# Kernel tuning notes

Measured on AMD Instinct MI355X. Metric: run time of the kernel, lower is better.

Reference implementation:

```python
import jax, jax.numpy as jnp
import numpy as np

N_EMBD = 512
N_HEAD = 8


def setup_inputs() -> dict:
    key = jax.random.key(0)
    k_x, k_aw, k_ab, k_pw, k_pb = jax.random.split(key, 5)
    B, T, E = 4, 2048, N_EMBD
    s = 1.0 / np.sqrt(E)
    return {
        "x": jax.random.normal(k_x, (B, T, E), dtype=jnp.float32),
        # torch Linear weight is [out, in]; store transposed for x @ W
        "c_attn_w": jax.random.uniform(k_aw, (E, 3 * E), jnp.float32, -s, s),
        "c_attn_b": jax.random.uniform(k_ab, (3 * E,), jnp.float32, -s, s),
        "c_proj_w": jax.random.uniform(k_pw, (E, E), jnp.float32, -s, s),
        "c_proj_b": jax.random.uniform(k_pb, (E,), jnp.float32, -s, s),
    }


def reference(x, c_attn_w, c_attn_b, c_proj_w, c_proj_b):
    B, T, E = x.shape
    H = N_HEAD
    D = E // H
    qkv = x @ c_attn_w + c_attn_b                      # [B,T,3E]
    q, k, v = jnp.split(qkv, 3, axis=2)
    # [B,T,E] -> [B,H,T,D]
    q = q.reshape(B, T, H, D).transpose(0, 2, 1, 3)
    k = k.reshape(B, T, H, D).transpose(0, 2, 1, 3)
    v = v.reshape(B, T, H, D).transpose(0, 2, 1, 3)
    scale = 1.0 / np.sqrt(D).astype(np.float32)
    scores = jnp.einsum("bhqd,bhkd->bhqk", q, k) * scale
    causal = jnp.tril(jnp.ones((T, T), dtype=bool))    # [T,T]
    scores = jnp.where(causal, scores, -jnp.inf)
    attn = jax.nn.softmax(scores, axis=-1)             # [B,H,T,T]
    y = jnp.einsum("bhqk,bhkd->bhqd", attn, v)         # [B,H,T,D]
    y = y.transpose(0, 2, 1, 3).reshape(B, T, E)
    return y @ c_proj_w + c_proj_b
```

## Files before the change

kernel.cpp:

```cpp
#include <hip/hip_runtime.h>
#include <math.h>

#define N_EMBD 512
#define N_HEAD 8
#define SEQ_T  2048
#define BATCH  4
#define QKV_LD 1536

typedef __attribute__((ext_vector_type(8))) short bf16x8;
typedef __attribute__((ext_vector_type(4))) float f32x4;

#define CL 0.18033688f

__device__ __forceinline__ unsigned short f2bf(float f) {
    union { float f; unsigned int u; } x; x.f = f;
    return (unsigned short)((x.u + 0x7FFFu + ((x.u >> 16) & 1u)) >> 16);
}
__device__ __forceinline__ unsigned pack_trunc(float a, float b) {
    union { float f; unsigned u; } x, y; x.f = a; y.f = b;
    return __builtin_amdgcn_perm(y.u, x.u, 0x07060302u);
}
__device__ __forceinline__ bf16x8 scale_frag(bf16x8 v, float c) {
    bf16x8 r;
    #pragma unroll
    for (int i = 0; i < 8; ++i) {
        union { unsigned u; float f; } x;
        x.u = ((unsigned)(unsigned short)v[i]) << 16;
        r[i] = (short)f2bf(x.f * c);
    }
    return r;
}

__device__ __forceinline__ void gl_lds16(const void* g, void* s) {
    __builtin_amdgcn_global_load_lds(
        (const __attribute__((address_space(1))) void*)g,
        (__attribute__((address_space(3))) void*)s, 16, 0, 0);
}

__global__ __launch_bounds__(256) void prep(
    const float* __restrict__ w1, unsigned short* __restrict__ w1t,
    const float* __restrict__ w2, unsigned short* __restrict__ w2t)
{
    __shared__ float t[32][33];
    const int bx = blockIdx.x, tid = threadIdx.x;
    const float* W; unsigned short* Wt; int N, tt, nb;
    if (bx < 768) { tt = bx;       W = w1; Wt = w1t; N = 1536; nb = 48; }
    else          { tt = bx - 768; W = w2; Wt = w2t; N = 512;  nb = 16; }
    const int n0 = (tt % nb) * 32, k0 = (tt / nb) * 32;
    const int tx = tid & 31, ty = tid >> 5;
    #pragma unroll
    for (int i = 0; i < 4; ++i)
        t[ty + i * 8][tx] = W[(size_t)(k0 + ty + i * 8) * N + n0 + tx];
    __syncthreads();
    #pragma unroll
    for (int i = 0; i < 4; ++i)
        Wt[(size_t)(n0 + ty + i * 8) * 512 + k0 + tx] = f2bf(t[tx][ty + i * 8]);
}

template <int BM, int BN, bool CVT_A, bool BF16_OUT>
__global__ __launch_bounds__(256) void gemm_mfma(
    const void* __restrict__ Asrc,
    const unsigned short* __restrict__ Bt,
    const float* __restrict__ bias,
    void* __restrict__ C, int N, int K)
{
    constexpr int WMT = BM / 32, WNT = BN / 32;
    constexpr int SA = BM * 8 / 256, SB = BN * 8 / 256;
    __shared__ unsigned short As[BM * 64];
    __shared__ unsigned short Bs[BN * 64];

    const int tid  = threadIdx.x;
    const int wave = tid >> 6, lane = tid & 63;
    const int low  = lane & 15, quad = lane >> 4;
    const int wm   = (wave & 1) * (BM / 2), wn = (wave >> 1) * (BN / 2);
    const int row0 = blockIdx.y * BM, col0 = blockIdx.x * BN;

    size_t a_src[SA]; int a_dst[SA];
    #pragma unroll
    for (int s = 0; s < SA; ++s) {
        const int p = tid + 256 * s;
        const int m = p >> 3, q = p & 7;
        a_src[s] = (size_t)(row0 + m) * K + q * 8;
        a_dst[s] = m * 64 + (q ^ (m & 7)) * 8;
    }
    size_t b_src[SB]; int b_dst[SB];
    #pragma unroll
    for (int s = 0; s < SB; ++s) {
        const int p = tid + 256 * s;
        const int m = p >> 3, q = p & 7;
        b_src[s] = (size_t)(col0 + m) * K + q * 8;
        b_dst[s] = m * 64 + (q ^ (m & 7)) * 8;
    }

    f32x4 acc[WMT][WNT];
    #pragma unroll
    for (int i = 0; i < WMT; ++i)
        #pragma unroll
        for (int j = 0; j < WNT; ++j) acc[i][j] = (f32x4){0.f, 0.f, 0.f, 0.f};

    bf16x8 ar[SA], br[SB];
    const float*          af32 = (const float*)Asrc;
    const unsigned short* a16  = (const unsigned short*)Asrc;

    #pragma unroll
    for (int s = 0; s < SA; ++s) {
        if (CVT_A) {
            const float4 f0 = *(const float4*)(af32 + a_src[s]);
            const float4 f1 = *(const float4*)(af32 + a_src[s] + 4);
            union { uint4 v; bf16x8 h; } u;
            u.v.x = pack_trunc(f0.x, f0.y); u.v.y = pack_trunc(f0.z, f0.w);
            u.v.z = pack_trunc(f1.x, f1.y); u.v.w = pack_trunc(f1.z, f1.w);
            ar[s] = u.h;
        } else {
            ar[s] = *(const bf16x8*)(a16 + a_src[s]);
        }
    }
    #pragma unroll
    for (int s = 0; s < SB; ++s) br[s] = *(const bf16x8*)(Bt + b_src[s]);

    const int NIT = K >> 6;
    for (int it = 0; it < NIT; ++it) {
        __syncthreads();
        #pragma unroll
        for (int s = 0; s < SA; ++s) *(bf16x8*)&As[a_dst[s]] = ar[s];
        #pragma unroll
        for (int s = 0; s < SB; ++s) *(bf16x8*)&Bs[b_dst[s]] = br[s];
        __syncthreads();

        if (it + 1 < NIT) {
            const int ko = (it + 1) * 64;
            #pragma unroll
            for (int s = 0; s < SA; ++s) {
                if (CVT_A) {
                    const float4 f0 = *(const float4*)(af32 + a_src[s] + ko);
                    const float4 f1 = *(const float4*)(af32 + a_src[s] + ko + 4);
                    union { uint4 v; bf16x8 h; } u;
                    u.v.x = pack_trunc(f0.x, f0.y); u.v.y = pack_trunc(f0.z, f0.w);
                    u.v.z = pack_trunc(f1.x, f1.y); u.v.w = pack_trunc(f1.z, f1.w);
                    ar[s] = u.h;
                } else {
                    ar[s] = *(const bf16x8*)(a16 + a_src[s] + ko);
                }
            }
            #pragma unroll
            for (int s = 0; s < SB; ++s) br[s] = *(const bf16x8*)(Bt + b_src[s] + ko);
        }

        #pragma unroll
        for (int h = 0; h < 2; ++h) {
            bf16x8 af[WMT], bfr[WNT];
            #pragma unroll
            for (int t = 0; t < WMT; ++t)
                af[t] = *(const bf16x8*)
                    &As[(wm + t * 16 + low) * 64 + (((h * 4 + quad) ^ (low & 7)) * 8)];
            #pragma unroll
            for (int t = 0; t < WNT; ++t)
                bfr[t] = *(const bf16x8*)
                    &Bs[(wn + t * 16 + low) * 64 + (((h * 4 + quad) ^ (low & 7)) * 8)];
            #pragma unroll
            for (int i = 0; i < WMT; ++i)
                #pragma unroll
                for (int j = 0; j < WNT; ++j)
                    acc[i][j] = __builtin_amdgcn_mfma_f32_16x16x32_bf16(
                        af[i], bfr[j], acc[i][j], 0, 0, 0);
        }
    }

    float bv[WNT];
    #pragma unroll
    for (int j = 0; j < WNT; ++j) bv[j] = bias[col0 + wn + j * 16 + low];
    #pragma unroll
    for (int i = 0; i < WMT; ++i)
        #pragma unroll
        for (int r = 0; r < 4; ++r) {
            const size_t row = row0 + wm + i * 16 + quad * 4 + r;
            #pragma unroll
            for (int j = 0; j < WNT; ++j) {
                const int col = col0 + wn + j * 16 + low;
                const float v = acc[i][j][r] + bv[j];
                if (BF16_OUT)
                    ((unsigned short*)C)[row * N + col] = f2bf(v);
                else
                    ((float*)C)[row * N + col] = v;
            }
        }
}

template <bool MASK>
__device__ __forceinline__ void tile_step(
    const bf16x8 kf[4][2], const bf16x8 qf0, const bf16x8 qf1,
    int thr, int quad, int low, unsigned short* ps)
{
    f32x4 s[4];
    #pragma unroll
    for (int st = 0; st < 4; ++st) {
        f32x4 a = (f32x4){0.f, 0.f, 0.f, 0.f};
        a = __builtin_amdgcn_mfma_f32_16x16x32_bf16(kf[st][0], qf0, a, 0, 0, 0);
        a = __builtin_amdgcn_mfma_f32_16x16x32_bf16(kf[st][1], qf1, a, 0, 0, 0);
        s[st] = a;
    }
    #pragma unroll
    for (int st = 0; st < 4; ++st) {
        float p[4];
        #pragma unroll
        for (int r = 0; r < 4; ++r) {
            float v = s[st][r];
            if (MASK) v = (st * 16 + r <= thr) ? v : -1e30f;
            p[r] = __builtin_amdgcn_exp2f(v);
        }
        uint2 pk;
        pk.x = pack_trunc(p[0], p[1]);
        pk.y = pack_trunc(p[2], p[3]);
        *(uint2*)&ps[low * 72 + st * 16 + quad * 4] = pk;
    }
}

__device__ __forceinline__ void pv_step(
    const bf16x8 vf[4][2], const unsigned short* ps, int quad, int low,
    f32x4* o, f32x4& lacc, const bf16x8 ones)
{
    const bf16x8 p0 = *(const bf16x8*)&ps[low * 72 + quad * 8];
    const bf16x8 p1 = *(const bf16x8*)&ps[low * 72 + quad * 8 + 32];
    #pragma unroll
    for (int t = 0; t < 4; ++t) {
        o[t] = __builtin_amdgcn_mfma_f32_16x16x32_bf16(p0, vf[t][0], o[t], 0, 0, 0);
        o[t] = __builtin_amdgcn_mfma_f32_16x16x32_bf16(p1, vf[t][1], o[t], 0, 0, 0);
    }
    lacc = __builtin_amdgcn_mfma_f32_16x16x32_bf16(p0, ones, lacc, 0, 0, 0);
    lacc = __builtin_amdgcn_mfma_f32_16x16x32_bf16(p1, ones, lacc, 0, 0, 0);
}

__global__ __launch_bounds__(256) void attn_mfma(
    const unsigned short* __restrict__ qkv,
    unsigned short* __restrict__ y)
{
    const int bh  = blockIdx.x & 31;
    const int pa  = blockIdx.x >> 5;
    const int b   = bh >> 3, h = bh & 7;
    const int qA0 = pa * 64;
    const int qB0 = (31 - pa) * 64;
    const int nA  = pa + 1, nB = 32 - pa;
    const int tid = threadIdx.x;
    const int wave = tid >> 6, lane = tid & 63;
    const int low  = lane & 15, quad = lane >> 4;

    __shared__ unsigned short Ks[2][64 * 64];
    __shared__ unsigned short Vt[2][64 * 64];
    __shared__ unsigned short PsA[4][16 * 72];
    __shared__ unsigned short PsB[4][16 * 72];

    const size_t base = (size_t)b * SEQ_T * QKV_LD + h * 64;
    const unsigned short* qp = qkv + base;
    const unsigned short* kp = qkv + base + 512;
    const unsigned short* vp = qkv + base + 1024;

    const int qmyA = qA0 + wave * 16 + low;
    const int qmyB = qB0 + wave * 16 + low;

    const bf16x8 qfA0 = scale_frag(*(const bf16x8*)(qp + (size_t)qmyA * QKV_LD + quad * 8), CL);
    const bf16x8 qfA1 = scale_frag(*(const bf16x8*)(qp + (size_t)qmyA * QKV_LD + quad * 8 + 32), CL);
    const bf16x8 qfB0 = scale_frag(*(const bf16x8*)(qp + (size_t)qmyB * QKV_LD + quad * 8), CL);
    const bf16x8 qfB1 = scale_frag(*(const bf16x8*)(qp + (size_t)qmyB * QKV_LD + quad * 8 + 32), CL);

    bf16x8 ones;
    #pragma unroll
    for (int i = 0; i < 8; ++i) ones[i] = (short)0x3F80;

    const int d0 = wave * 8;
    unsigned short* psA = &PsA[wave][0];
    unsigned short* psB = &PsB[wave][0];

    bf16x8 vr0 = *(const bf16x8*)(vp + (size_t)lane * QKV_LD + d0);
    bf16x8 vr1 = *(const bf16x8*)(vp + (size_t)lane * QKV_LD + d0 + 32);
    {
        #pragma unroll
        for (int ii = 0; ii < 2; ++ii) {
            const int row = wave * 16 + ii * 8 + (lane >> 3);
            const int o   = (lane & 7) ^ (lane >> 3);
            gl_lds16(kp + (size_t)row * QKV_LD + o * 8, &Ks[0][(wave * 2 + ii) * 512]);
        }
        #pragma unroll
        for (int ii = 0; ii < 8; ++ii) {
            const int po = ((lane >> 3) ^ ii) * 8 + (lane & 7);
            Vt[0][((d0 + ii) << 6) + po]      = (unsigned short)vr0[ii];
            Vt[0][((d0 + 32 + ii) << 6) + po] = (unsigned short)vr1[ii];
        }
        if (nB > 1) {
            vr0 = *(const bf16x8*)(vp + (size_t)(64 + lane) * QKV_LD + d0);
            vr1 = *(const bf16x8*)(vp + (size_t)(64 + lane) * QKV_LD + d0 + 32);
        }
    }
    __syncthreads();

    f32x4 oA[4], oB[4], lA, lB;
    #pragma unroll
    for (int t = 0; t < 4; ++t) {
        oA[t] = (f32x4){0.f, 0.f, 0.f, 0.f};
        oB[t] = (f32x4){0.f, 0.f, 0.f, 0.f};
    }
    lA = (f32x4){0.f, 0.f, 0.f, 0.f};
    lB = (f32x4){0.f, 0.f, 0.f, 0.f};

    for (int kc = 0; kc < nB; ++kc) {
        const int cur = kc & 1;
        unsigned short* ksc = &Ks[cur][0];
        unsigned short* vtc = &Vt[cur][0];

        if (kc + 1 < nB) {
            const int key1 = (kc + 1) * 64;
            #pragma unroll
            for (int ii = 0; ii < 2; ++ii) {
                const int row = wave * 16 + ii * 8 + (lane >> 3);
                const int o   = (lane & 7) ^ (lane >> 3);
                gl_lds16(kp + (size_t)(key1 + row) * QKV_LD + o * 8,
                         &Ks[cur ^ 1][(wave * 2 + ii) * 512]);
            }
            unsigned short* vtn = &Vt[cur ^ 1][0];
            #pragma unroll
            for (int ii = 0; ii < 8; ++ii) {
                const int po = ((lane >> 3) ^ ii) * 8 + (lane & 7);
                vtn[((d0 + ii) << 6) + po]      = (unsigned short)vr0[ii];
                vtn[((d0 + 32 + ii) << 6) + po] = (unsigned short)vr1[ii];
            }
        }
        if (kc + 2 < nB) {
            const int key2 = (kc + 2) * 64;
            vr0 = *(const bf16x8*)(vp + (size_t)(key2 + lane) * QKV_LD + d0);
            vr1 = *(const bf16x8*)(vp + (size_t)(key2 + lane) * QKV_LD + d0 + 32);
        }

        const int key0 = kc * 64;
        bf16x8 kf[4][2];
        #pragma unroll
        for (int t = 0; t < 4; ++t)
            #pragma unroll
            for (int i = 0; i < 2; ++i)
                kf[t][i] = *(const bf16x8*)
                    &ksc[((t * 16 + low) << 6) + (((quad + 4 * i) ^ (low & 7)) << 3)];

        if (kc < nA) {
            if (kc == nA - 1)
                tile_step<true >(kf, qfA0, qfA1, qmyA - key0 - quad * 4, quad, low, psA);
            else
                tile_step<false>(kf, qfA0, qfA1, 0, quad, low, psA);
        }
        if (kc == nB - 1)
            tile_step<true >(kf, qfB0, qfB1, qmyB - key0 - quad * 4, quad, low, psB);
        else
            tile_step<false>(kf, qfB0, qfB1, 0, quad, low, psB);

        asm volatile("" ::: "memory");

        bf16x8 vf[4][2];
        #pragma unroll
        for (int t = 0; t < 4; ++t)
            #pragma unroll
            for (int i = 0; i < 2; ++i)
                vf[t][i] = *(const bf16x8*)
                    &vtc[((t * 16 + low) << 6) + (((quad + 4 * i) ^ (low & 7)) << 3)];

        if (kc < nA) pv_step(vf, psA, quad, low, oA, lA, ones);
        pv_step(vf, psB, quad, low, oB, lB, ones);
        __syncthreads();
    }

    #pragma unroll
    for (int r = 0; r < 4; ++r) {
        const float rlA = 1.f / lA[r];
        const int qrow = qA0 + wave * 16 + quad * 4 + r;
        unsigned short* yp = y + (size_t)(b * SEQ_T + qrow) * N_EMBD + h * 64 + low;
        #pragma unroll
        for (int t = 0; t < 4; ++t) yp[16 * t] = f2bf(oA[t][r] * rlA);
    }
    #pragma unroll
    for (int r = 0; r < 4; ++r) {
        const float rlB = 1.f / lB[r];
        const int qrow = qB0 + wave * 16 + quad * 4 + r;
        unsigned short* yp = y + (size_t)(b * SEQ_T + qrow) * N_EMBD + h * 64 + low;
        #pragma unroll
        for (int t = 0; t < 4; ++t) yp[16 * t] = f2bf(oB[t][r] * rlB);
    }
}

extern "C" void kernel_launch(void* const* d_in, const int* in_sizes, int n_in,
                              void* d_out, int out_size, void* d_ws, size_t ws_size,
                              hipStream_t stream)
{
    const float* x      = (const float*)d_in[0];
    const float* attn_w = (const float*)d_in[1];
    const float* attn_b = (const float*)d_in[2];
    const float* proj_w = (const float*)d_in[3];
    const float* proj_b = (const float*)d_in[4];
    float*       out    = (float*)d_out;

    char* ws = (char*)d_ws;
    unsigned short* qkv_bf = (unsigned short*)(ws);
    unsigned short* y_bf   = (unsigned short*)(ws + 25165824);
    unsigned short* w1t    = (unsigned short*)(ws + 33554432);
    unsigned short* w2t    = (unsigned short*)(ws + 35127296);

    prep<<<1024, 256, 0, stream>>>(attn_w, w1t, proj_w, w2t);

    gemm_mfma<128, 128, true, true><<<dim3(12, 64), 256, 0, stream>>>(
        x, w1t, attn_b, qkv_bf, QKV_LD, N_EMBD);

    attn_mfma<<<dim3(512), 256, 0, stream>>>(qkv_bf, y_bf);

    gemm_mfma<64, 128, false, false><<<dim3(4, 128), 256, 0, stream>>>(
        y_bf, w2t, proj_b, out, N_EMBD, N_EMBD);
}
```

Before: 152.2 us.

## Fuse all stages into one persistent kernel with grid-wide barriers

Replaces the four separate launches (weight prep, QKV GEMM, attention, projection GEMM) with a single 512-block persistent kernel that runs each stage in turn, separated by atomic-counter grid barriers, and shares LDS through a union. The intent is to remove launch gaps and tail drain between kernels. The QKV GEMM now uses 64x128 tiles with an XCD-aware tile mapping instead of 128x128 tiles. This relies on all 512 blocks being co-resident, which launch_bounds(256,2) and the LDS usage must allow; otherwise it deadlocks. It also adds barrier spin overhead and a memset launch.

```diff
diff --git a/kernel.cpp b/kernel.cpp
--- a/kernel.cpp
+++ b/kernel.cpp
@@ -6,6 +6,7 @@
 #define SEQ_T  2048
 #define BATCH  4
 #define QKV_LD 1536
+#define NBLK   512
 
 typedef __attribute__((ext_vector_type(8))) short bf16x8;
 typedef __attribute__((ext_vector_type(4))) float f32x4;
@@ -30,50 +31,58 @@
     }
     return r;
 }
-
 __device__ __forceinline__ void gl_lds16(const void* g, void* s) {
     __builtin_amdgcn_global_load_lds(
         (const __attribute__((address_space(1))) void*)g,
         (__attribute__((address_space(3))) void*)s, 16, 0, 0);
 }
 
-__global__ __launch_bounds__(256) void prep(
+struct AttnSh { unsigned short Ks[2][4096], Vt[2][4096], PsA[4][1152], PsB[4][1152]; };
+struct GemmSh { unsigned short As[4096], Bs[8192]; };
+struct PrepSh { float t[32][33]; };
+union SharedU { AttnSh a; GemmSh g; PrepSh p; };
+
+__device__ __forceinline__ void grid_sync(int* bar) {
+    __syncthreads();
+    if (threadIdx.x == 0) {
+        __hip_atomic_fetch_add(bar, 1, __ATOMIC_ACQ_REL, __HIP_MEMORY_SCOPE_AGENT);
+        while (__hip_atomic_load(bar, __ATOMIC_ACQUIRE, __HIP_MEMORY_SCOPE_AGENT) < NBLK)
+            __builtin_amdgcn_s_sleep(2);
+    }
+    __syncthreads();
+}
+
+__device__ __forceinline__ void prep_tile(
+    PrepSh& sp, int job,
     const float* __restrict__ w1, unsigned short* __restrict__ w1t,
-    const float* __restrict__ w2, unsigned short* __restrict__ w2t)
-{
-    __shared__ float t[32][33];
-    const int bx = blockIdx.x, tid = threadIdx.x;
+    const float* __restrict__ w2, unsigned short* __restrict__ w2t, int tid)
+{
     const float* W; unsigned short* Wt; int N, tt, nb;
-    if (bx < 768) { tt = bx;       W = w1; Wt = w1t; N = 1536; nb = 48; }
-    else          { tt = bx - 768; W = w2; Wt = w2t; N = 512;  nb = 16; }
+    if (job < 768) { tt = job;       W = w1; Wt = w1t; N = 1536; nb = 48; }
+    else           { tt = job - 768; W = w2; Wt = w2t; N = 512;  nb = 16; }
     const int n0 = (tt % nb) * 32, k0 = (tt / nb) * 32;
     const int tx = tid & 31, ty = tid >> 5;
     #pragma unroll
     for (int i = 0; i < 4; ++i)
-        t[ty + i * 8][tx] = W[(size_t)(k0 + ty + i * 8) * N + n0 + tx];
+        sp.t[ty + i * 8][tx] = W[(size_t)(k0 + ty + i * 8) * N + n0 + tx];
     __syncthreads();
     #pragma unroll
     for (int i = 0; i < 4; ++i)
-        Wt[(size_t)(n0 + ty + i * 8) * 512 + k0 + tx] = f2bf(t[tx][ty + i * 8]);
-}
-
-template <int BM, int BN, bool CVT_A, bool BF16_OUT>
-__global__ __launch_bounds__(256) void gemm_mfma(
-    const void* __restrict__ Asrc,
-    const unsigned short* __restrict__ Bt,
-    const float* __restrict__ bias,
-    void* __restrict__ C, int N, int K)
-{
-    constexpr int WMT = BM / 32, WNT = BN / 32;
-    constexpr int SA = BM * 8 / 256, SB = BN * 8 / 256;
-    __shared__ unsigned short As[BM * 64];
-    __shared__ unsigned short Bs[BN * 64];
-
-    const int tid  = threadIdx.x;
+        Wt[(size_t)(n0 + ty + i * 8) * 512 + k0 + tx] = f2bf(sp.t[tx][ty + i * 8]);
+    __syncthreads();
+}
+
+template <bool CVT_A, bool BF16_OUT>
+__device__ __forceinline__ void gemm_tile(
+    GemmSh& sg, const void* __restrict__ Asrc,
+    const unsigned short* __restrict__ Bt, const float* __restrict__ bias,
+    void* __restrict__ C, int N, int row0, int col0, int tid)
+{
+    constexpr int K = 512;
+    constexpr int WMT = 2, WNT = 4, SA = 2, SB = 4;
     const int wave = tid >> 6, lane = tid & 63;
     const int low  = lane & 15, quad = lane >> 4;
-    const int wm   = (wave & 1) * (BM / 2), wn = (wave >> 1) * (BN / 2);
-    const int row0 = blockIdx.y * BM, col0 = blockIdx.x * BN;
+    const int wm   = (wave & 1) * 32, wn = (wave >> 1) * 64;
 
     size_t a_src[SA]; int a_dst[SA];
     #pragma unroll
@@ -122,9 +131,9 @@
     for (int it = 0; it < NIT; ++it) {
         __syncthreads();
         #pragma unroll
-        for (int s = 0; s < SA; ++s) *(bf16x8*)&As[a_dst[s]] = ar[s];
-        #pragma unroll
-        for (int s = 0; s < SB; ++s) *(bf16x8*)&Bs[b_dst[s]] = br[s];
+        for (int s = 0; s < SA; ++s) *(bf16x8*)&sg.As[a_dst[s]] = ar[s];
+        #pragma unroll
+        for (int s = 0; s < SB; ++s) *(bf16x8*)&sg.Bs[b_dst[s]] = br[s];
         __syncthreads();
 
         if (it + 1 < NIT) {
@@ -152,11 +161,11 @@
             #pragma unroll
             for (int t = 0; t < WMT; ++t)
                 af[t] = *(const bf16x8*)
-                    &As[(wm + t * 16 + low) * 64 + (((h * 4 + quad) ^ (low & 7)) * 8)];
+                    &sg.As[(wm + t * 16 + low) * 64 + (((h * 4 + quad) ^ (low & 7)) * 8)];
             #pragma unroll
             for (int t = 0; t < WNT; ++t)
                 bfr[t] = *(const bf16x8*)
-                    &Bs[(wn + t * 16 + low) * 64 + (((h * 4 + quad) ^ (low & 7)) * 8)];
+                    &sg.Bs[(wn + t * 16 + low) * 64 + (((h * 4 + quad) ^ (low & 7)) * 8)];
             #pragma unroll
             for (int i = 0; i < WMT; ++i)
                 #pragma unroll
@@ -165,6 +174,7 @@
                         af[i], bfr[j], acc[i][j], 0, 0, 0);
         }
     }
+    __syncthreads();
 
     float bv[WNT];
     #pragma unroll
@@ -230,24 +240,18 @@
     lacc = __builtin_amdgcn_mfma_f32_16x16x32_bf16(p1, ones, lacc, 0, 0, 0);
 }
 
-__global__ __launch_bounds__(256) void attn_mfma(
-    const unsigned short* __restrict__ qkv,
-    unsigned short* __restrict__ y)
-{
-    const int bh  = blockIdx.x & 31;
-    const int pa  = blockIdx.x >> 5;
+__device__ __forceinline__ void attn_block(
+    AttnSh& sa, int id,
+    const unsigned short* __restrict__ qkv, unsigned short* __restrict__ y, int tid)
+{
+    const int bh  = id & 31;
+    const int pa  = id >> 5;
     const int b   = bh >> 3, h = bh & 7;
     const int qA0 = pa * 64;
     const int qB0 = (31 - pa) * 64;
     const int nA  = pa + 1, nB = 32 - pa;
-    const int tid = threadIdx.x;
     const int wave = tid >> 6, lane = tid & 63;
     const int low  = lane & 15, quad = lane >> 4;
-
-    __shared__ unsigned short Ks[2][64 * 64];
-    __shared__ unsigned short Vt[2][64 * 64];
-    __shared__ unsigned short PsA[4][16 * 72];
-    __shared__ unsigned short PsB[4][16 * 72];
 
     const size_t base = (size_t)b * SEQ_T * QKV_LD + h * 64;
     const unsigned short* qp = qkv + base;
@@ -267,8 +271,8 @@
     for (int i = 0; i < 8; ++i) ones[i] = (short)0x3F80;
 
     const int d0 = wave * 8;
-    unsigned short* psA = &PsA[wave][0];
-    unsigned short* psB = &PsB[wave][0];
+    unsigned short* psA = &sa.PsA[wave][0];
+    unsigned short* psB = &sa.PsB[wave][0];
 
     bf16x8 vr0 = *(const bf16x8*)(vp + (size_t)lane * QKV_LD + d0);
     bf16x8 vr1 = *(const bf16x8*)(vp + (size_t)lane * QKV_LD + d0 + 32);
@@ -277,13 +281,13 @@
         for (int ii = 0; ii < 2; ++ii) {
             const int row = wave * 16 + ii * 8 + (lane >> 3);
             const int o   = (lane & 7) ^ (lane >> 3);
-            gl_lds16(kp + (size_t)row * QKV_LD + o * 8, &Ks[0][(wave * 2 + ii) * 512]);
+            gl_lds16(kp + (size_t)row * QKV_LD + o * 8, &sa.Ks[0][(wave * 2 + ii) * 512]);
         }
         #pragma unroll
         for (int ii = 0; ii < 8; ++ii) {
             const int po = ((lane >> 3) ^ ii) * 8 + (lane & 7);
-            Vt[0][((d0 + ii) << 6) + po]      = (unsigned short)vr0[ii];
-            Vt[0][((d0 + 32 + ii) << 6) + po] = (unsigned short)vr1[ii];
+            sa.Vt[0][((d0 + ii) << 6) + po]      = (unsigned short)vr0[ii];
+            sa.Vt[0][((d0 + 32 + ii) << 6) + po] = (unsigned short)vr1[ii];
         }
         if (nB > 1) {
             vr0 = *(const bf16x8*)(vp + (size_t)(64 + lane) * QKV_LD + d0);
@@ -303,8 +307,8 @@
 
     for (int kc = 0; kc < nB; ++kc) {
         const int cur = kc & 1;
-        unsigned short* ksc = &Ks[cur][0];
-        unsigned short* vtc = &Vt[cur][0];
+        unsigned short* ksc = &sa.Ks[cur][0];
+        unsigned short* vtc = &sa.Vt[cur][0];
 
         if (kc + 1 < nB) {
             const int key1 = (kc + 1) * 64;
@@ -313,9 +317,9 @@
                 const int row = wave * 16 + ii * 8 + (lane >> 3);
                 const int o   = (lane & 7) ^ (lane >> 3);
                 gl_lds16(kp + (size_t)(key1 + row) * QKV_LD + o * 8,
-                         &Ks[cur ^ 1][(wave * 2 + ii) * 512]);
+                         &sa.Ks[cur ^ 1][(wave * 2 + ii) * 512]);
             }
-            unsigned short* vtn = &Vt[cur ^ 1][0];
+            unsigned short* vtn = &sa.Vt[cur ^ 1][0];
             #pragma unroll
             for (int ii = 0; ii < 8; ++ii) {
                 const int po = ((lane >> 3) ^ ii) * 8 + (lane & 7);
@@ -379,6 +383,46 @@
         unsigned short* yp = y + (size_t)(b * SEQ_T + qrow) * N_EMBD + h * 64 + low;
         #pragma unroll
         for (int t = 0; t < 4; ++t) yp[16 * t] = f2bf(oB[t][r] * rlB);
+    }
+}
+
+__global__ __launch_bounds__(256, 2) void mega(
+    const float* __restrict__ x,
+    const float* __restrict__ w1, const float* __restrict__ b1,
+    const float* __restrict__ w2, const float* __restrict__ b2,
+    float* __restrict__ out,
+    unsigned short* __restrict__ qkv, unsigned short* __restrict__ ybf,
+    unsigned short* __restrict__ w1t, unsigned short* __restrict__ w2t,
+    int* __restrict__ bars)
+{
+    __shared__ SharedU sh;
+    const int id  = blockIdx.x;
+    const int tid = threadIdx.x;
+
+    prep_tile(sh.p, id,       w1, w1t, w2, w2t, tid);
+    prep_tile(sh.p, id + 512, w1, w1t, w2, w2t, tid);
+    grid_sync(&bars[0]);
+
+    #pragma unroll
+    for (int j = 0; j < 3; ++j) {
+        const int job    = id + NBLK * j;
+        const int xcd    = job & 7;
+        const int within = job >> 3;
+        const int row0   = (xcd * 16 + (within & 15)) * 64;
+        const int col0   = (within >> 4) * 128;
+        gemm_tile<true, true>(sh.g, x, w1t, b1, qkv, QKV_LD, row0, col0, tid);
+    }
+    grid_sync(&bars[1]);
+
+    attn_block(sh.a, id, qkv, ybf, tid);
+    grid_sync(&bars[2]);
+
+    {
+        const int xcd    = id & 7;
+        const int within = id >> 3;
+        const int row0   = (xcd * 16 + (within & 15)) * 64;
+        const int col0   = (within >> 4) * 128;
+        gemm_tile<false, false>(sh.g, ybf, w2t, b2, out, N_EMBD, row0, col0, tid);
     }
 }
 
@@ -398,14 +442,11 @@
     unsigned short* y_bf   = (unsigned short*)(ws + 25165824);
     unsigned short* w1t    = (unsigned short*)(ws + 33554432);
     unsigned short* w2t    = (unsigned short*)(ws + 35127296);
-
-    prep<<<1024, 256, 0, stream>>>(attn_w, w1t, proj_w, w2t);
-
-    gemm_mfma<128, 128, true, true><<<dim3(12, 64), 256, 0, stream>>>(
-        x, w1t, attn_b, qkv_bf, QKV_LD, N_EMBD);
-
-    attn_mfma<<<dim3(512), 256, 0, stream>>>(qkv_bf, y_bf);
-
-    gemm_mfma<64, 128, false, false><<<dim3(4, 128), 256, 0, stream>>>(
-        y_bf, w2t, proj_b, out, N_EMBD, N_EMBD);
-}
+    int*            bars   = (int*)(ws + 35651584);
+
+    hipMemsetAsync(bars, 0, 64, stream);
+
+    mega<<<dim3(NBLK), 256, 0, stream>>>(
+        x, attn_w, attn_b, proj_w, proj_b, out,
+        qkv_bf, y_bf, w1t, w2t, bars);
+}
```

After: 376.8 us. +147.5%, slower.
